# Optimization experiments

Hardware: AMD Instinct MI355X
Metric: run time of the kernel (lower is better)

The kernel has to match this reference:

```python
import jax, jax.numpy as jnp
import numpy as np

B, S, D = 2, 2048, 1024
H, DQK, DV = 16, 64, 64

def setup_inputs() -> dict:
    key = jax.random.key(0)
    k1, k2, k3, k4, k5 = jax.random.split(key, 5)
    scale_in = 1.0 / np.sqrt(D)
    scale_v = 1.0 / np.sqrt(H * DV)
    return {
        "x":   jax.random.normal(k1, (B, S, D), dtype=jnp.float32),
        "W_q": jax.random.uniform(k2, (D, H * DQK), minval=-scale_in, maxval=scale_in, dtype=jnp.float32),
        "W_k": jax.random.uniform(k3, (D, H * DQK), minval=-scale_in, maxval=scale_in, dtype=jnp.float32),
        "W_v": jax.random.uniform(k4, (D, H * DV), minval=-scale_in, maxval=scale_in, dtype=jnp.float32),
        "W_o": jax.random.uniform(k5, (H * DV, D), minval=-scale_v, maxval=scale_v, dtype=jnp.float32),
    }

def reference(x, W_q, W_k, W_v, W_o):
    b, s, _ = x.shape
    # projections -> [B, H, S, d]
    Q = (x @ W_q).reshape(b, s, H, DQK).transpose(0, 2, 1, 3)
    K = (x @ W_k).reshape(b, s, H, DQK).transpose(0, 2, 1, 3)
    V = (x @ W_v).reshape(b, s, H, DV).transpose(0, 2, 1, 3)
    scores = jnp.einsum('bhqd,bhkd->bhqk', Q, K) / np.sqrt(DQK).astype(np.float32)
    causal_mask = jnp.triu(jnp.ones((s, s), dtype=bool), k=1)  # True above diagonal
    scores = jnp.where(causal_mask[None, None], -jnp.inf, scores)
    attn = jax.nn.softmax(scores, axis=-1)
    out = jnp.einsum('bhqk,bhkd->bhqd', attn, V)  # [B,H,S,DV]
    out = out.transpose(0, 2, 1, 3).reshape(b, s, H * DV)
    return out @ W_o
```

## Files before the change

### kernel.cpp

```cpp
#include <hip/hip_runtime.h>


typedef float  f32x4  __attribute__((ext_vector_type(4)));
typedef __bf16 bf16x8 __attribute__((ext_vector_type(8)));

__device__ __forceinline__ unsigned short f2bf(float f) {
    __bf16 h = (__bf16)f;
    return __builtin_bit_cast(unsigned short, h);
}

__device__ __forceinline__ void gld16(unsigned short* lds, const unsigned short* g) {
    __builtin_amdgcn_global_load_lds(
        (const __attribute__((address_space(1))) void*)g,
        (__attribute__((address_space(3))) void*)lds, 16, 0, 0);
}

__global__ __launch_bounds__(256) void castx(const float* __restrict__ x,
                                             unsigned short* __restrict__ xb) {
    size_t i = ((size_t)blockIdx.x * 256 + threadIdx.x) * 4;
    float4 v = *(const float4*)(x + i);
    ushort4 o;
    o.x = f2bf(v.x); o.y = f2bf(v.y); o.z = f2bf(v.z); o.w = f2bf(v.w);
    *(ushort4*)(xb + i) = o;
}

__global__ __launch_bounds__(256) void wtrans(const float* __restrict__ W0,
                                              const float* __restrict__ W1,
                                              const float* __restrict__ W2,
                                              const float* __restrict__ W3,
                                              unsigned short* __restrict__ WT) {
    __shared__ float T[64][65];
    const int z = blockIdx.z;
    const float* W = (z == 0) ? W0 : (z == 1) ? W1 : (z == 2) ? W2 : W3;
    const int k0 = blockIdx.y * 64, n0 = blockIdx.x * 64;
    const int tid = threadIdx.x;
#pragma unroll
    for (int i = 0; i < 4; i++) {
        int c = tid + i * 256;
        int r = c >> 4, col = (c & 15) * 4;
        float4 v = *(const float4*)(W + (size_t)(k0 + r) * 1024 + n0 + col);
        T[r][col] = v.x; T[r][col + 1] = v.y; T[r][col + 2] = v.z; T[r][col + 3] = v.w;
    }
    __syncthreads();
    unsigned short* out = WT + (size_t)z * 1024 * 1024;
#pragma unroll
    for (int i = 0; i < 2; i++) {
        int c = tid + i * 256;
        int nr = c >> 3, koff = (c & 7) * 8;
        union { unsigned short us[8]; uint4 v; } pk;
#pragma unroll
        for (int j = 0; j < 8; j++) pk.us[j] = f2bf(T[koff + j][nr]);
        *(uint4*)(out + (size_t)(n0 + nr) * 1024 + k0 + koff) = pk.v;
    }
}

__global__ __launch_bounds__(256) void gemm_qkv(const unsigned short* __restrict__ A,
                                                const unsigned short* __restrict__ WTall,
                                                unsigned short* __restrict__ outq,
                                                unsigned short* __restrict__ Vp) {
    __shared__ unsigned short As0[128 * 64];
    __shared__ unsigned short Bs0[128 * 64];
    __shared__ unsigned short As1[128 * 64];
    __shared__ unsigned short Bs1[128 * 64];
    const int tid = threadIdx.x;
    const int w = tid >> 6, lane = tid & 63, quad = lane >> 4, ln = lane & 15;

    const int blk = blockIdx.x;
    const int n0 = ((blk >> 3) & 7) * 128;
    const int g  = ((blk >> 6) << 3) | (blk & 7);
    const int z  = g >> 5;
    const int m0 = (g & 31) * 128;

    const unsigned short* BT = WTall + (size_t)z * (1024 * 1024);
    const float scl = (z == 0) ? 0.180336878f : 1.0f;
    const bool swp = (z < 2);

    const int lr8 = lane >> 3;
    const int lc8 = ((lane & 7) ^ lr8) * 8;
    const int fsw = (quad ^ (ln & 7)) * 8;

    const f32x4 z4 = {0.f, 0.f, 0.f, 0.f};
    f32x4 acc[4][4];
#pragma unroll
    for (int i = 0; i < 4; i++)
#pragma unroll
        for (int j = 0; j < 4; j++) acc[i][j] = z4;

    const int wm = (w & 1) * 64, wn = (w >> 1) * 64;
    const int Rb = w * 32;

#define QKV_STAGE(Ad, Bd, kk)                                                              \
    {                                                                                      \
        _Pragma("unroll")                                                                  \
        for (int s = 0; s < 4; s++) {                                                      \
            gld16(Ad + (Rb + s * 8) * 64, A  + (size_t)(m0 + Rb + s * 8 + lr8) * 1024 + (kk) + lc8); \
            gld16(Bd + (Rb + s * 8) * 64, BT + (size_t)(n0 + Rb + s * 8 + lr8) * 1024 + (kk) + lc8); \
        }                                                                                  \
    }

#define QKV_COMPUTE(Ad, Bd)                                                                \
    {                                                                                      \
        _Pragma("unroll")                                                                  \
        for (int ks = 0; ks < 2; ks++) {                                                   \
            const int co = fsw ^ (ks * 32);                                                \
            bf16x8 af[4], bfr[4];                                                          \
            _Pragma("unroll")                                                              \
            for (int t = 0; t < 4; t++)                                                    \
                af[t] = *(const bf16x8*)&Ad[(wm + t * 16 + ln) * 64 + co];                 \
            _Pragma("unroll")                                                              \
            for (int t = 0; t < 4; t++)                                                    \
                bfr[t] = *(const bf16x8*)&Bd[(wn + t * 16 + ln) * 64 + co];                \
            if (swp) {                                                                     \
                _Pragma("unroll")                                                          \
                for (int tm = 0; tm < 4; tm++)                                             \
                    _Pragma("unroll")                                                      \
                    for (int tn = 0; tn < 4; tn++)                                         \
                        acc[tm][tn] = __builtin_amdgcn_mfma_f32_16x16x32_bf16(             \
                            bfr[tn], af[tm], acc[tm][tn], 0, 0, 0);                        \
            } else {                                                                       \
                _Pragma("unroll")                                                          \
                for (int tm = 0; tm < 4; tm++)                                             \
                    _Pragma("unroll")                                                      \
                    for (int tn = 0; tn < 4; tn++)                                         \
                        acc[tm][tn] = __builtin_amdgcn_mfma_f32_16x16x32_bf16(             \
                            af[tm], bfr[tn], acc[tm][tn], 0, 0, 0);                        \
            }                                                                              \
        }                                                                                  \
    }

    QKV_STAGE(As0, Bs0, 0);
    for (int k0 = 0; k0 < 1024; k0 += 128) {
        __syncthreads();
        if (k0 + 64 < 1024) QKV_STAGE(As1, Bs1, k0 + 64);
        QKV_COMPUTE(As0, Bs0);
        __syncthreads();
        if (k0 + 128 < 1024) QKV_STAGE(As0, Bs0, k0 + 128);
        if (k0 + 64 < 1024) QKV_COMPUTE(As1, Bs1);
    }
#undef QKV_STAGE
#undef QKV_COMPUTE

    if (swp) {
#pragma unroll
        for (int tm = 0; tm < 4; tm++)
#pragma unroll
            for (int tn = 0; tn < 4; tn++) {
                int mg = m0 + wm + tm * 16 + ln;
                int nb = n0 + wn + tn * 16 + quad * 4;
                int b = mg >> 11, s = mg & 2047, h = nb >> 6, dd = nb & 63;
                ushort4 o;
                o.x = f2bf(acc[tm][tn][0] * scl);
                o.y = f2bf(acc[tm][tn][1] * scl);
                o.z = f2bf(acc[tm][tn][2] * scl);
                o.w = f2bf(acc[tm][tn][3] * scl);
                size_t zoff = (size_t)z * (4096 * 1024);
                *(ushort4*)(outq + zoff + (((size_t)(b * 16 + h) * 2048 + s) << 6) + dd) = o;
            }
    } else {
#pragma unroll
        for (int tm = 0; tm < 4; tm++)
#pragma unroll
            for (int tn = 0; tn < 4; tn++) {
                int mg = m0 + wm + tm * 16 + quad * 4;
                int ng = n0 + wn + tn * 16 + ln;
                int b = mg >> 11, h = ng >> 6, dd = ng & 63;
                int sblk = (mg & 2047) & ~63;
                int cb = tm >> 1, t16 = tm & 1;
                int pp = cb * 32 + quad * 8 + t16 * 4;
                ushort4 o;
                o.x = f2bf(acc[tm][tn][0]);
                o.y = f2bf(acc[tm][tn][1]);
                o.z = f2bf(acc[tm][tn][2]);
                o.w = f2bf(acc[tm][tn][3]);
                *(ushort4*)(Vp + ((size_t)(b * 16 + h) * 64 + dd) * 2048 + sblk + pp) = o;
            }
    }
}

__global__ __launch_bounds__(256) void gemm_o(const unsigned short* __restrict__ A,
                                              const unsigned short* __restrict__ BT,
                                              float* __restrict__ outf) {
    __shared__ unsigned short As0[128 * 64];
    __shared__ unsigned short Bs0[128 * 64];
    __shared__ unsigned short As1[128 * 64];
    __shared__ unsigned short Bs1[128 * 64];
    const int tid = threadIdx.x;
    const int w = tid >> 6, lane = tid & 63, quad = lane >> 4, ln = lane & 15;

    const int blk = blockIdx.x;
    const int n0 = ((blk >> 3) & 7) * 128;
    const int m0 = (((blk >> 6) << 3) | (blk & 7)) * 128;

    const int lr8 = lane >> 3;
    const int lc8 = ((lane & 7) ^ lr8) * 8;
    const int fsw = (quad ^ (ln & 7)) * 8;

    const f32x4 z4 = {0.f, 0.f, 0.f, 0.f};
    f32x4 acc[4][4];
#pragma unroll
    for (int i = 0; i < 4; i++)
#pragma unroll
        for (int j = 0; j < 4; j++) acc[i][j] = z4;

    const int wm = (w & 1) * 64, wn = (w >> 1) * 64;
    const int Rb = w * 32;

#define O_STAGE(Ad, Bd, kk)                                                                \
    {                                                                                      \
        _Pragma("unroll")                                                                  \
        for (int s = 0; s < 4; s++) {                                                      \
            gld16(Ad + (Rb + s * 8) * 64, A  + (size_t)(m0 + Rb + s * 8 + lr8) * 1024 + (kk) + lc8); \
            gld16(Bd + (Rb + s * 8) * 64, BT + (size_t)(n0 + Rb + s * 8 + lr8) * 1024 + (kk) + lc8); \
        }                                                                                  \
    }

#define O_COMPUTE(Ad, Bd)                                                                  \
    {                                                                                      \
        _Pragma("unroll")                                                                  \
        for (int ks = 0; ks < 2; ks++) {                                                   \
            const int co = fsw ^ (ks * 32);                                                \
            bf16x8 af[4], bfr[4];                                                          \
            _Pragma("unroll")                                                              \
            for (int t = 0; t < 4; t++)                                                    \
                af[t] = *(const bf16x8*)&Ad[(wm + t * 16 + ln) * 64 + co];                 \
            _Pragma("unroll")                                                              \
            for (int t = 0; t < 4; t++)                                                    \
                bfr[t] = *(const bf16x8*)&Bd[(wn + t * 16 + ln) * 64 + co];                \
            _Pragma("unroll")                                                              \
            for (int tm = 0; tm < 4; tm++)                                                 \
                _Pragma("unroll")                                                          \
                for (int tn = 0; tn < 4; tn++)                                             \
                    acc[tm][tn] = __builtin_amdgcn_mfma_f32_16x16x32_bf16(                 \
                        bfr[tn], af[tm], acc[tm][tn], 0, 0, 0);                            \
        }                                                                                  \
    }

    O_STAGE(As0, Bs0, 0);
    for (int k0 = 0; k0 < 1024; k0 += 128) {
        __syncthreads();
        if (k0 + 64 < 1024) O_STAGE(As1, Bs1, k0 + 64);
        O_COMPUTE(As0, Bs0);
        __syncthreads();
        if (k0 + 128 < 1024) O_STAGE(As0, Bs0, k0 + 128);
        if (k0 + 64 < 1024) O_COMPUTE(As1, Bs1);
    }
#undef O_STAGE
#undef O_COMPUTE

#pragma unroll
    for (int tm = 0; tm < 4; tm++)
#pragma unroll
        for (int tn = 0; tn < 4; tn++) {
            int mg = m0 + wm + tm * 16 + ln;
            int nb = n0 + wn + tn * 16 + quad * 4;
            *(f32x4*)(outf + (size_t)mg * 1024 + nb) = acc[tm][tn];
        }
}

__global__ __launch_bounds__(512, 4) void flash(const unsigned short* __restrict__ Qb,
                                                const unsigned short* __restrict__ Kb,
                                                const unsigned short* __restrict__ Vpb,
                                                unsigned short* __restrict__ AO,
                                                float* __restrict__ Ph0,
                                                float* __restrict__ Ph1,
                                                float* __restrict__ Lb) {
    __shared__ __align__(16) unsigned short Ks[2][64 * 64];
    __shared__ __align__(16) unsigned short Vs[2][64 * 64];
    const int tid = threadIdx.x, w = tid >> 6, lane = tid & 63;
    const int qd = lane >> 4, ln = lane & 15;
    const int lr = lane >> 3;
    const int lchunk = (lane & 7) ^ lr;
    const int psw = (qd ^ (ln & 7)) * 8;

    const int blk = blockIdx.x;
    const int bh = blk & 31;
    const int s  = blk >> 5;
    int qi, kstart, kend, half;
    bool heavy;
    if (s < 8) {
        qi = s; kstart = 0; kend = (qi + 1) * 128; half = 0; heavy = false;
    } else {
        int t = s - 8; half = t >> 3; qi = 15 - (t & 7); heavy = true;
        int mid = (qi + 1) * 64;
        kstart = half ? mid : 0;
        kend   = half ? (qi + 1) * 128 : mid;
    }
    const int qt0 = qi * 128;

    const unsigned short* Kg = Kb  + (size_t)bh * 2048 * 64;
    const unsigned short* Vg = Vpb + (size_t)bh * 64 * 2048;

    bf16x8 aq[2];
    {
        const unsigned short* Qrow = Qb + ((size_t)bh * 2048 + qt0 + w * 16 + ln) * 64 + qd * 8;
        aq[0] = *(const bf16x8*)(Qrow);
        aq[1] = *(const bf16x8*)(Qrow + 32);
    }

    const f32x4 z4 = {0.f, 0.f, 0.f, 0.f};
    f32x4 Oc[4];
#pragma unroll
    for (int td = 0; td < 4; td++) Oc[td] = z4;
    float lsum = 0.f;

    const int qrow = qt0 + w * 16 + ln;
    const int qmin = qt0 + w * 16;
    const int qmax = qmin + 15;

#define FLASH_STAGE(buf, kk)                                                          \
    {                                                                                 \
        const unsigned short* kg = Kg + (size_t)((kk) + w * 8 + lr) * 64 + lchunk * 8; \
        gld16(&Ks[buf][(w * 8) * 64], kg);                                            \
        const unsigned short* vg = Vg + (size_t)(w * 8 + lr) * 2048 + (kk) + lchunk * 8; \
        gld16(&Vs[buf][(w * 8) * 64], vg);                                            \
    }

    FLASH_STAGE(0, kstart);
    int cur = 0;

    for (int k0 = kstart; k0 < kend; k0 += 64) {
        __syncthreads();
        if (k0 + 64 < kend) FLASH_STAGE(cur ^ 1, k0 + 64);

        if (k0 <= qmax) {
            f32x4 sc[4];
#pragma unroll
            for (int t = 0; t < 4; t++) {
                sc[t] = z4;
                if (k0 + t * 16 <= qmax) {
                    int off = (t * 16 + ln) * 64 + psw;
                    bf16x8 bk0 = *(const bf16x8*)&Ks[cur][off];
                    bf16x8 bk1 = *(const bf16x8*)&Ks[cur][off ^ 32];
                    sc[t] = __builtin_amdgcn_mfma_f32_16x16x32_bf16(bk0, aq[0], sc[t], 0, 0, 0);
                    sc[t] = __builtin_amdgcn_mfma_f32_16x16x32_bf16(bk1, aq[1], sc[t], 0, 0, 0);
                }
            }

            unsigned int pk[4][2];
#pragma unroll
            for (int t = 0; t < 4; t++) {
                if (k0 + t * 16 > qmax) { pk[t][0] = 0u; pk[t][1] = 0u; continue; }
                float e[4];
#pragma unroll
                for (int r2 = 0; r2 < 4; r2++) e[r2] = __builtin_amdgcn_exp2f(sc[t][r2]);
                if (k0 + t * 16 + 15 > qmin) {
#pragma unroll
                    for (int r2 = 0; r2 < 4; r2++)
                        if (k0 + t * 16 + qd * 4 + r2 > qrow) e[r2] = 0.f;
                }
                lsum += (e[0] + e[1]) + (e[2] + e[3]);
                pk[t][0] = (unsigned int)f2bf(e[0]) | ((unsigned int)f2bf(e[1]) << 16);
                pk[t][1] = (unsigned int)f2bf(e[2]) | ((unsigned int)f2bf(e[3]) << 16);
            }

            union { unsigned int u[4]; bf16x8 v; } apu0, apu1;
            apu0.u[0] = pk[0][0]; apu0.u[1] = pk[0][1]; apu0.u[2] = pk[1][0]; apu0.u[3] = pk[1][1];
            apu1.u[0] = pk[2][0]; apu1.u[1] = pk[2][1]; apu1.u[2] = pk[3][0]; apu1.u[3] = pk[3][1];
#pragma unroll
            for (int td = 0; td < 4; td++) {
                int voff = (td * 16 + ln) * 64 + psw;
                bf16x8 av0 = *(const bf16x8*)&Vs[cur][voff];
                bf16x8 av1 = *(const bf16x8*)&Vs[cur][voff ^ 32];
                Oc[td] = __builtin_amdgcn_mfma_f32_16x16x32_bf16(av0, apu0.v, Oc[td], 0, 0, 0);
                Oc[td] = __builtin_amdgcn_mfma_f32_16x16x32_bf16(av1, apu1.v, Oc[td], 0, 0, 0);
            }
        }
        cur ^= 1;
    }
#undef FLASH_STAGE

    lsum += __shfl_xor(lsum, 16);
    lsum += __shfl_xor(lsum, 32);

    if (!heavy) {
        const float inv = 1.0f / lsum;
        const int bz = bh >> 4, h = bh & 15;
        const int rowg = qt0 + w * 16 + ln;
        unsigned short* aorow = AO + ((size_t)(bz * 2048 + rowg) << 10) + h * 64 + qd * 4;
#pragma unroll
        for (int td = 0; td < 4; td++) {
            ushort4 o;
            o.x = f2bf(Oc[td][0] * inv);
            o.y = f2bf(Oc[td][1] * inv);
            o.z = f2bf(Oc[td][2] * inv);
            o.w = f2bf(Oc[td][3] * inv);
            *(ushort4*)(aorow + td * 16) = o;
        }
    } else {
        float* P = half ? Ph1 : Ph0;
        const int prow = ((bh * 8 + (qi - 8)) * 128) + w * 16 + ln;
        float* Pr = P + (size_t)prow * 64 + qd * 4;
#pragma unroll
        for (int td = 0; td < 4; td++)
            *(f32x4*)(Pr + td * 16) = Oc[td];
        if (qd == 0) Lb[half * 32768 + prow] = lsum;
    }
}

__global__ __launch_bounds__(256) void merge(const float* __restrict__ P0,
                                             const float* __restrict__ P1,
                                             const float* __restrict__ Lb,
                                             unsigned short* __restrict__ AO) {
    const int idx = blockIdx.x * 256 + threadIdx.x;
    const int d0 = (idx & 7) * 8;
    const int row = idx >> 3;
    const float inv = 1.0f / (Lb[row] + Lb[32768 + row]);
    const float* a = P0 + (size_t)row * 64 + d0;
    const float* b = P1 + (size_t)row * 64 + d0;
    f32x4 x0 = *(const f32x4*)a, x1 = *(const f32x4*)(a + 4);
    f32x4 y0 = *(const f32x4*)b, y1 = *(const f32x4*)(b + 4);
    union { unsigned short us[8]; uint4 v; } pk;
#pragma unroll
    for (int j = 0; j < 4; j++) {
        pk.us[j]     = f2bf((x0[j] + y0[j]) * inv);
        pk.us[j + 4] = f2bf((x1[j] + y1[j]) * inv);
    }
    const int bh = row >> 10, qi8 = (row >> 7) & 7, q = row & 127;
    const int bz = bh >> 4, h = bh & 15;
    const int rowg = (qi8 + 8) * 128 + q;
    *(uint4*)(AO + ((size_t)(bz * 2048 + rowg) << 10) + h * 64 + d0) = pk.v;
}

extern "C" void kernel_launch(void* const* d_in, const int* in_sizes, int n_in,
                              void* d_out, int out_size, void* d_ws, size_t ws_size,
                              hipStream_t stream) {
    const float* x  = (const float*)d_in[0];
    const float* Wq = (const float*)d_in[1];
    const float* Wk = (const float*)d_in[2];
    const float* Wv = (const float*)d_in[3];
    const float* Wo = (const float*)d_in[4];
    float* out = (float*)d_out;

    unsigned short* xb  = (unsigned short*)d_ws;
    unsigned short* WT  = xb  + (size_t)4096 * 1024;
    unsigned short* Qb  = WT  + (size_t)4 * 1024 * 1024;
    unsigned short* Kb  = Qb  + (size_t)4096 * 1024;
    unsigned short* Vb  = Kb  + (size_t)4096 * 1024;
    unsigned short* Vpb = Vb  + (size_t)4096 * 1024;
    unsigned short* AO  = Vpb + (size_t)4096 * 1024;

    float* Ph0 = (float*)Vb;
    float* Ph1 = (float*)xb;
    float* Lb  = (float*)WT;

    castx<<<4096, 256, 0, stream>>>(x, xb);
    wtrans<<<dim3(16, 16, 4), 256, 0, stream>>>(Wq, Wk, Wv, Wo, WT);
    gemm_qkv<<<dim3(768), 256, 0, stream>>>(xb, WT, Qb, Vpb);
    flash<<<dim3(768), 512, 0, stream>>>(Qb, Kb, Vpb, AO, Ph0, Ph1, Lb);
    merge<<<dim3(1024), 256, 0, stream>>>(Ph0, Ph1, Lb, AO);
    gemm_o<<<dim3(256), 256, 0, stream>>>(AO, WT + (size_t)3 * 1024 * 1024, out);
}
```

Baseline: 170.1 us.

## Fuse split-KV merge into output GEMM, merge prep kernels, add MFMA priority hints

Removes the separate merge kernel. The output projection GEMM now reads the two fp32 partial attention outputs and the row sums directly for the heavy query rows, normalizes them, converts to bf16 and writes them into LDS. The cast and weight-transpose kernels are merged into one launch, and the flash kernel raises wave priority around its MFMA blocks. This saves two launches and one round trip of the AO write/read, at the cost of extra fp32 global traffic and register use inside the GEMM. Heavy row tiles also fall back to synchronous register loads instead of async LDS loads.

```diff
diff --git a/kernel.cpp b/kernel.cpp
--- a/kernel.cpp
+++ b/kernel.cpp
@@ -15,25 +15,28 @@
         (__attribute__((address_space(3))) void*)lds, 16, 0, 0);
 }
 
-__global__ __launch_bounds__(256) void castx(const float* __restrict__ x,
-                                             unsigned short* __restrict__ xb) {
-    size_t i = ((size_t)blockIdx.x * 256 + threadIdx.x) * 4;
-    float4 v = *(const float4*)(x + i);
-    ushort4 o;
-    o.x = f2bf(v.x); o.y = f2bf(v.y); o.z = f2bf(v.z); o.w = f2bf(v.w);
-    *(ushort4*)(xb + i) = o;
-}
-
-__global__ __launch_bounds__(256) void wtrans(const float* __restrict__ W0,
-                                              const float* __restrict__ W1,
-                                              const float* __restrict__ W2,
-                                              const float* __restrict__ W3,
-                                              unsigned short* __restrict__ WT) {
+__global__ __launch_bounds__(256) void prep(const float* __restrict__ x,
+                                            const float* __restrict__ W0,
+                                            const float* __restrict__ W1,
+                                            const float* __restrict__ W2,
+                                            const float* __restrict__ W3,
+                                            unsigned short* __restrict__ xb,
+                                            unsigned short* __restrict__ WT) {
     __shared__ float T[64][65];
-    const int z = blockIdx.z;
+    const int blk = blockIdx.x;
+    const int tid = threadIdx.x;
+    if (blk < 4096) {
+        size_t i = ((size_t)blk * 256 + tid) * 4;
+        float4 v = *(const float4*)(x + i);
+        ushort4 o;
+        o.x = f2bf(v.x); o.y = f2bf(v.y); o.z = f2bf(v.z); o.w = f2bf(v.w);
+        *(ushort4*)(xb + i) = o;
+        return;
+    }
+    const int t = blk - 4096;
+    const int z = t >> 8;
+    const int k0 = ((t >> 4) & 15) * 64, n0 = (t & 15) * 64;
     const float* W = (z == 0) ? W0 : (z == 1) ? W1 : (z == 2) ? W2 : W3;
-    const int k0 = blockIdx.y * 64, n0 = blockIdx.x * 64;
-    const int tid = threadIdx.x;
 #pragma unroll
     for (int i = 0; i < 4; i++) {
         int c = tid + i * 256;
@@ -179,6 +182,9 @@
 
 __global__ __launch_bounds__(256) void gemm_o(const unsigned short* __restrict__ A,
                                               const unsigned short* __restrict__ BT,
+                                              const float* __restrict__ P0,
+                                              const float* __restrict__ P1,
+                                              const float* __restrict__ Lb,
                                               float* __restrict__ outf) {
     __shared__ unsigned short As0[128 * 64];
     __shared__ unsigned short Bs0[128 * 64];
@@ -195,6 +201,17 @@
     const int lc8 = ((lane & 7) ^ lr8) * 8;
     const int fsw = (quad ^ (ln & 7)) * 8;
 
+    const bool heavyA = (m0 >> 10) & 1;
+    const int wm = (w & 1) * 64, wn = (w >> 1) * 64;
+    const int Rb = w * 32;
+
+    int rb[4];
+#pragma unroll
+    for (int s = 0; s < 4; s++) {
+        int r = m0 + Rb + s * 8 + lr8;
+        rb[s] = ((r >> 11) << 14) + (r & 2047) - 1024;
+    }
+
     const f32x4 z4 = {0.f, 0.f, 0.f, 0.f};
     f32x4 acc[4][4];
 #pragma unroll
@@ -202,16 +219,49 @@
 #pragma unroll
         for (int j = 0; j < 4; j++) acc[i][j] = z4;
 
-    const int wm = (w & 1) * 64, wn = (w >> 1) * 64;
-    const int Rb = w * 32;
-
-#define O_STAGE(Ad, Bd, kk)                                                                \
+    f32x4 ar[4][4];
+    float inv[4];
+
+#define A_LOAD(kk)                                                                         \
+    if (heavyA) {                                                                          \
+        const int hh = (kk) >> 6;                                                          \
+        _Pragma("unroll")                                                                  \
+        for (int s = 0; s < 4; s++) {                                                      \
+            const int rp = rb[s] + hh * 1024;                                              \
+            const float* p0 = P0 + (size_t)rp * 64 + lc8;                                  \
+            const float* p1 = P1 + (size_t)rp * 64 + lc8;                                  \
+            ar[s][0] = *(const f32x4*)p0;  ar[s][1] = *(const f32x4*)(p0 + 4);             \
+            ar[s][2] = *(const f32x4*)p1;  ar[s][3] = *(const f32x4*)(p1 + 4);             \
+            inv[s] = 1.0f / (Lb[rp] + Lb[32768 + rp]);                                     \
+        }                                                                                  \
+    }
+
+#define A_WRITE(Ad)                                                                        \
+    if (heavyA) {                                                                          \
+        _Pragma("unroll")                                                                  \
+        for (int s = 0; s < 4; s++) {                                                      \
+            union { unsigned short us[8]; uint4 v; } pk;                                   \
+            _Pragma("unroll")                                                              \
+            for (int j = 0; j < 4; j++) {                                                  \
+                pk.us[j]     = f2bf((ar[s][0][j] + ar[s][2][j]) * inv[s]);                 \
+                pk.us[j + 4] = f2bf((ar[s][1][j] + ar[s][3][j]) * inv[s]);                 \
+            }                                                                              \
+            *(uint4*)&Ad[(Rb + s * 8) * 64 + lane * 8] = pk.v;                             \
+        }                                                                                  \
+    }
+
+#define A_GLD(Ad, kk)                                                                      \
+    if (!heavyA) {                                                                         \
+        _Pragma("unroll")                                                                  \
+        for (int s = 0; s < 4; s++)                                                        \
+            gld16(Ad + (Rb + s * 8) * 64, A + (size_t)(m0 + Rb + s * 8 + lr8) * 1024 + (kk) + lc8); \
+    }
+
+#define B_GLD(Bd, kk)                                                                      \
     {                                                                                      \
         _Pragma("unroll")                                                                  \
-        for (int s = 0; s < 4; s++) {                                                      \
-            gld16(Ad + (Rb + s * 8) * 64, A  + (size_t)(m0 + Rb + s * 8 + lr8) * 1024 + (kk) + lc8); \
+        for (int s = 0; s < 4; s++)                                                        \
             gld16(Bd + (Rb + s * 8) * 64, BT + (size_t)(n0 + Rb + s * 8 + lr8) * 1024 + (kk) + lc8); \
-        }                                                                                  \
     }
 
 #define O_COMPUTE(Ad, Bd)                                                                  \
@@ -235,16 +285,21 @@
         }                                                                                  \
     }
 
-    O_STAGE(As0, Bs0, 0);
+    A_LOAD(0); A_GLD(As0, 0); B_GLD(Bs0, 0); A_WRITE(As0);
     for (int k0 = 0; k0 < 1024; k0 += 128) {
         __syncthreads();
-        if (k0 + 64 < 1024) O_STAGE(As1, Bs1, k0 + 64);
+        if (k0 + 64 < 1024) { A_LOAD(k0 + 64); A_GLD(As1, k0 + 64); B_GLD(Bs1, k0 + 64); }
         O_COMPUTE(As0, Bs0);
+        if (k0 + 64 < 1024) A_WRITE(As1);
         __syncthreads();
-        if (k0 + 128 < 1024) O_STAGE(As0, Bs0, k0 + 128);
+        if (k0 + 128 < 1024) { A_LOAD(k0 + 128); A_GLD(As0, k0 + 128); B_GLD(Bs0, k0 + 128); }
         if (k0 + 64 < 1024) O_COMPUTE(As1, Bs1);
-    }
-#undef O_STAGE
+        if (k0 + 128 < 1024) A_WRITE(As0);
+    }
+#undef A_LOAD
+#undef A_WRITE
+#undef A_GLD
+#undef B_GLD
 #undef O_COMPUTE
 
 #pragma unroll
@@ -324,6 +379,7 @@
 
         if (k0 <= qmax) {
             f32x4 sc[4];
+            __builtin_amdgcn_s_setprio(1);
 #pragma unroll
             for (int t = 0; t < 4; t++) {
                 sc[t] = z4;
@@ -335,6 +391,7 @@
                     sc[t] = __builtin_amdgcn_mfma_f32_16x16x32_bf16(bk1, aq[1], sc[t], 0, 0, 0);
                 }
             }
+            __builtin_amdgcn_s_setprio(0);
 
             unsigned int pk[4][2];
 #pragma unroll
@@ -356,6 +413,7 @@
             union { unsigned int u[4]; bf16x8 v; } apu0, apu1;
             apu0.u[0] = pk[0][0]; apu0.u[1] = pk[0][1]; apu0.u[2] = pk[1][0]; apu0.u[3] = pk[1][1];
             apu1.u[0] = pk[2][0]; apu1.u[1] = pk[2][1]; apu1.u[2] = pk[3][0]; apu1.u[3] = pk[3][1];
+            __builtin_amdgcn_s_setprio(1);
 #pragma unroll
             for (int td = 0; td < 4; td++) {
                 int voff = (td * 16 + ln) * 64 + psw;
@@ -364,6 +422,7 @@
                 Oc[td] = __builtin_amdgcn_mfma_f32_16x16x32_bf16(av0, apu0.v, Oc[td], 0, 0, 0);
                 Oc[td] = __builtin_amdgcn_mfma_f32_16x16x32_bf16(av1, apu1.v, Oc[td], 0, 0, 0);
             }
+            __builtin_amdgcn_s_setprio(0);
         }
         cur ^= 1;
     }
@@ -397,30 +456,6 @@
     }
 }
 
-__global__ __launch_bounds__(256) void merge(const float* __restrict__ P0,
-                                             const float* __restrict__ P1,
-                                             const float* __restrict__ Lb,
-                                             unsigned short* __restrict__ AO) {
-    const int idx = blockIdx.x * 256 + threadIdx.x;
-    const int d0 = (idx & 7) * 8;
-    const int row = idx >> 3;
-    const float inv = 1.0f / (Lb[row] + Lb[32768 + row]);
-    const float* a = P0 + (size_t)row * 64 + d0;
-    const float* b = P1 + (size_t)row * 64 + d0;
-    f32x4 x0 = *(const f32x4*)a, x1 = *(const f32x4*)(a + 4);
-    f32x4 y0 = *(const f32x4*)b, y1 = *(const f32x4*)(b + 4);
-    union { unsigned short us[8]; uint4 v; } pk;
-#pragma unroll
-    for (int j = 0; j < 4; j++) {
-        pk.us[j]     = f2bf((x0[j] + y0[j]) * inv);
-        pk.us[j + 4] = f2bf((x1[j] + y1[j]) * inv);
-    }
-    const int bh = row >> 10, qi8 = (row >> 7) & 7, q = row & 127;
-    const int bz = bh >> 4, h = bh & 15;
-    const int rowg = (qi8 + 8) * 128 + q;
-    *(uint4*)(AO + ((size_t)(bz * 2048 + rowg) << 10) + h * 64 + d0) = pk.v;
-}
-
 extern "C" void kernel_launch(void* const* d_in, const int* in_sizes, int n_in,
                               void* d_out, int out_size, void* d_ws, size_t ws_size,
                               hipStream_t stream) {
@@ -443,10 +478,8 @@
     float* Ph1 = (float*)xb;
     float* Lb  = (float*)WT;
 
-    castx<<<4096, 256, 0, stream>>>(x, xb);
-    wtrans<<<dim3(16, 16, 4), 256, 0, stream>>>(Wq, Wk, Wv, Wo, WT);
+    prep<<<dim3(5120), 256, 0, stream>>>(x, Wq, Wk, Wv, Wo, xb, WT);
     gemm_qkv<<<dim3(768), 256, 0, stream>>>(xb, WT, Qb, Vpb);
     flash<<<dim3(768), 512, 0, stream>>>(Qb, Kb, Vpb, AO, Ph0, Ph1, Lb);
-    merge<<<dim3(1024), 256, 0, stream>>>(Ph0, Ph1, Lb, AO);
-    gemm_o<<<dim3(256), 256, 0, stream>>>(AO, WT + (size_t)3 * 1024 * 1024, out);
-}
+    gemm_o<<<dim3(256), 256, 0, stream>>>(AO, WT + (size_t)3 * 1024 * 1024, Ph0, Ph1, Lb, out);
+}
```

Result: slower. 174.8 us (+2.8%).
